# Optimization experiments

Hardware: AMD Instinct MI355X
Metric: run time of the kernel (lower is better)

The kernel has to match this reference:

```python
import jax, jax.numpy as jnp
import numpy as np

NUM_HOPS = 3

def _position_encoding(sentence_size, embedding_size):
    # Vectorized version of the double loop in the source.
    i = np.arange(1, embedding_size + 1, dtype=np.float32)[:, None]  # [E,1]
    j = np.arange(1, sentence_size + 1, dtype=np.float32)[None, :]   # [1,S]
    enc = (i - embedding_size / 2.0) * (j - sentence_size / 2.0)
    enc = 1.0 + 4.0 * enc / embedding_size / sentence_size
    return jnp.asarray(np.transpose(enc))  # [S, E]

def setup_inputs() -> dict:
    key = jax.random.key(0)
    ks = jax.random.split(key, 9)
    B, M, S, E, V, OUT = 16, 512, 32, 128, 32000, 128
    scale = 0.02
    return {
        "queries": jax.random.randint(ks[0], (B, S), 0, V, dtype=jnp.int32),
        "stories": jax.random.randint(ks[1], (B, M, S), 0, V, dtype=jnp.int32),
        "query_biases": jax.random.normal(ks[2], (V - 1, E), jnp.float32) * scale,
        "stories_biases": jax.random.normal(ks[3], (V - 1, E), jnp.float32) * scale,
        "memory_biases": jax.random.normal(ks[4], (M, E), jnp.float32) * scale,
        "output_biases": jax.random.normal(ks[5], (V - 1, E), jnp.float32) * scale,
        "w_intermediate": jax.random.normal(ks[6], (E, E), jnp.float32) * scale,
        "w_output": jax.random.normal(ks[7], (E, OUT), jnp.float32) * scale,
        "w_final": jax.random.normal(ks[8], (OUT, V), jnp.float32) * scale,
    }

def reference(queries, stories, query_biases, stories_biases, memory_biases,
              output_biases, w_intermediate, w_output, w_final):
    B, M, S = stories.shape
    E = query_biases.shape[1]
    enc = _position_encoding(S, E)  # [S, E]
    nil = jnp.zeros((1, E), dtype=query_biases.dtype)

    # Story memory: gather -> positional weight -> reduce over sentence axis.
    st_tab = jnp.concatenate([stories_biases, nil], axis=0)          # [V, E]
    mem_emb = st_tab[stories]                                        # [B,M,S,E]
    memory = jnp.einsum('bmse,se->bme', mem_emb, enc) + memory_biases

    # Query embedding.
    q_tab = jnp.concatenate([query_biases, nil], axis=0)
    q = jnp.einsum('bse,se->be', q_tab[queries], enc)                # [B,E]

    # Output memory.
    o_tab = jnp.concatenate([output_biases, nil], axis=0)
    output = jnp.einsum('bmse,se->bme', o_tab[stories], enc)         # [B,M,E]

    out_layer = q
    for hop in range(NUM_HOPS):
        probs = jax.nn.softmax(jnp.einsum('bme,be->bm', memory, q))  # [B,M]
        layer_out = jnp.einsum('bme,bm->be', output, probs)          # [B,E]
        w = w_output if hop == NUM_HOPS - 1 else w_intermediate
        out_layer = (q + layer_out) @ w
        q = out_layer                     # pre-nonlinearity state, as in source
        out_layer = jax.nn.relu(out_layer)

    return out_layer @ w_final            # [B, vocab]
```

## Files before the change

### kernel.cpp

```cpp
#include <hip/hip_runtime.h>

constexpr int kB  = 16;
constexpr int kM  = 512;
constexpr int kS  = 32;
constexpr int kE  = 128;
constexpr int kV  = 32000;
constexpr int kVN = kV - 1;

__global__ __launch_bounds__(256) void embed_stories_kernel(
    const int*   __restrict__ stories,
    const float* __restrict__ st_bias,
    const float* __restrict__ out_bias,
    const float* __restrict__ mem_bias,
    float*       __restrict__ memory,
    float*       __restrict__ output)
{
    __shared__ int sidx[2][kS];
    const int t     = threadIdx.x;
    const int pair0 = blockIdx.x * 2;
    if (t < 64) {
        const int p = t >> 5, s = t & 31;
        sidx[p][s] = stories[(pair0 + p) * kS + s];
    }
    __syncthreads();
    const int p  = t >> 7;
    const int e  = t & 127;
    const int bm = pair0 + p;
    const int m  = bm & (kM - 1);

    float accm = mem_bias[m * kE + e];
    float acco = 0.0f;
    const float ef = (float)(e - 63);
    #pragma unroll
    for (int s = 0; s < kS; ++s) {
        const int idx   = sidx[p][s];
        const float enc = 1.0f + ef * (float)(s - 15) * (1.0f / 1024.0f);
        if (idx < kVN) {
            const size_t off = (size_t)idx * kE + e;
            accm = fmaf(st_bias[off],  enc, accm);
            acco = fmaf(out_bias[off], enc, acco);
        }
    }
    memory[(size_t)bm * kE + e] = accm;
    output[(size_t)bm * kE + e] = acco;
}

__global__ __launch_bounds__(512) void hops_kernel(
    const int*   __restrict__ queries,
    const float* __restrict__ q_bias,
    const float* __restrict__ memory,
    const float* __restrict__ output,
    const float* __restrict__ w_int,
    const float* __restrict__ w_out,
    float*       __restrict__ x)
{
    __shared__ __align__(16) float q_s[kE];
    __shared__ float xbuf[kE];
    __shared__ float sc[kM];
    __shared__ float part[4][kE];
    __shared__ float red[8];
    __shared__ int   qidx[kS];

    const int b = blockIdx.x;
    const int t = threadIdx.x;

    if (t < kS) qidx[t] = queries[b * kS + t];
    __syncthreads();

    if (t < kE) {
        float acc = 0.0f;
        const float ef = (float)(t - 63);
        #pragma unroll
        for (int s = 0; s < kS; ++s) {
            const int idx   = qidx[s];
            const float enc = 1.0f + ef * (float)(s - 15) * (1.0f / 1024.0f);
            if (idx < kVN) acc = fmaf(q_bias[(size_t)idx * kE + t], enc, acc);
        }
        q_s[t] = acc;
    }
    __syncthreads();

    const float* memb = memory + (size_t)b * kM * kE;
    const float* outb = output + (size_t)b * kM * kE;
    const int g = t >> 7;
    const int e = t & 127;

    for (int hop = 0; hop < 3; ++hop) {
        const float4* row = (const float4*)(memb + (size_t)t * kE);
        const float4* qv  = (const float4*)q_s;
        float sv = 0.0f;
        #pragma unroll
        for (int i = 0; i < kE / 4; ++i) {
            const float4 a = row[i], q4 = qv[i];
            sv += a.x * q4.x + a.y * q4.y + a.z * q4.z + a.w * q4.w;
        }
        float v = sv;
        #pragma unroll
        for (int off = 32; off; off >>= 1) v = fmaxf(v, __shfl_down(v, off, 64));
        if ((t & 63) == 0) red[t >> 6] = v;
        __syncthreads();
        float mx = red[0];
        #pragma unroll
        for (int i = 1; i < 8; ++i) mx = fmaxf(mx, red[i]);
        const float ex = __expf(sv - mx);
        float sum = ex;
        #pragma unroll
        for (int off = 32; off; off >>= 1) sum += __shfl_down(sum, off, 64);
        __syncthreads();
        if ((t & 63) == 0) red[t >> 6] = sum;
        sc[t] = ex;
        __syncthreads();
        const float tot = red[0] + red[1] + red[2] + red[3] +
                          red[4] + red[5] + red[6] + red[7];
        const float inv = 1.0f / tot;

        float acc = 0.0f;
        const float* ob = outb + (size_t)g * 128 * kE;
        for (int mm = 0; mm < 128; ++mm)
            acc = fmaf(sc[g * 128 + mm], ob[(size_t)mm * kE + e], acc);
        part[g][e] = acc;
        __syncthreads();
        if (t < kE) {
            const float lo = (part[0][t] + part[1][t] + part[2][t] + part[3][t]) * inv;
            xbuf[t] = q_s[t] + lo;
        }
        __syncthreads();

        const float* w = (hop == 2) ? w_out : w_int;
        float acc2 = 0.0f;
        #pragma unroll 4
        for (int k = 0; k < 32; ++k) {
            const int ee = g * 32 + k;
            acc2 = fmaf(xbuf[ee], w[ee * kE + e], acc2);
        }
        part[g][e] = acc2;
        __syncthreads();
        if (t < kE) q_s[t] = part[0][t] + part[1][t] + part[2][t] + part[3][t];
        __syncthreads();
    }
    if (t < kE) x[b * kE + t] = fmaxf(q_s[t], 0.0f);
}

__global__ __launch_bounds__(256) void final_mm_kernel(
    const float* __restrict__ x,
    const float* __restrict__ wf,
    float*       __restrict__ out)
{
    __shared__ float xs[kB * kE];
    const int t = threadIdx.x;
    for (int i = t; i < kB * kE; i += 256) xs[i] = x[i];
    __syncthreads();

    const int v  = blockIdx.x * 256 + t;
    const int e0 = blockIdx.y * 32;
    float acc[kB];
    #pragma unroll
    for (int b = 0; b < kB; ++b) acc[b] = 0.0f;
    for (int e = e0; e < e0 + 32; ++e) {
        const float w = wf[(size_t)e * kV + v];
        #pragma unroll
        for (int b = 0; b < kB; ++b) acc[b] = fmaf(xs[b * kE + e], w, acc[b]);
    }
    #pragma unroll
    for (int b = 0; b < kB; ++b) atomicAdd(&out[(size_t)b * kV + v], acc[b]);
}

extern "C" void kernel_launch(void* const* d_in, const int* in_sizes, int n_in,
                              void* d_out, int out_size, void* d_ws, size_t ws_size,
                              hipStream_t stream)
{
    const int*   queries  = (const int*)  d_in[0];
    const int*   stories  = (const int*)  d_in[1];
    const float* q_bias   = (const float*)d_in[2];
    const float* st_bias  = (const float*)d_in[3];
    const float* mem_bias = (const float*)d_in[4];
    const float* out_bias = (const float*)d_in[5];
    const float* w_int    = (const float*)d_in[6];
    const float* w_out    = (const float*)d_in[7];
    const float* w_final  = (const float*)d_in[8];
    float* out = (float*)d_out;

    float* memory = (float*)d_ws;
    float* output = memory + (size_t)kB * kM * kE;
    float* x      = output + (size_t)kB * kM * kE;

    hipMemsetAsync(d_out, 0, (size_t)out_size * sizeof(float), stream);

    embed_stories_kernel<<<dim3((kB * kM) / 2), dim3(256), 0, stream>>>(
        stories, st_bias, out_bias, mem_bias, memory, output);

    hops_kernel<<<dim3(kB), dim3(512), 0, stream>>>(
        queries, q_bias, memory, output, w_int, w_out, x);

    final_mm_kernel<<<dim3(kV / 256, 4), dim3(256), 0, stream>>>(x, w_final, out);
}
```

Measured before the change: 186.2 us.

## Fuse hops and final matmul into one cooperative kernel; vectorize embedding gathers

The embedding kernel now has each warp gather float4 slices of eight sentence positions, with a shared-memory reduction across positions. The hops and final projection are merged into one cooperative launch of 256 blocks. Each of the 16 batches is computed redundantly by 16 blocks, a grid sync follows, and then each block computes 125 vocab columns over the full E dimension. This removes the memset, the atomics and one launch. The cost is redundant hop work, a grid-wide barrier, and a final matmul that uses only 125 of 256 threads per block.

```diff
diff --git a/kernel.cpp b/kernel.cpp
--- a/kernel.cpp
+++ b/kernel.cpp
@@ -1,4 +1,7 @@
 #include <hip/hip_runtime.h>
+#include <hip/hip_cooperative_groups.h>
+
+namespace cg = cooperative_groups;
 
 constexpr int kB  = 16;
 constexpr int kM  = 512;
@@ -16,153 +19,211 @@
     float*       __restrict__ output)
 {
     __shared__ int sidx[2][kS];
-    const int t     = threadIdx.x;
-    const int pair0 = blockIdx.x * 2;
-    if (t < 64) {
-        const int p = t >> 5, s = t & 31;
-        sidx[p][s] = stories[(pair0 + p) * kS + s];
-    }
-    __syncthreads();
-    const int p  = t >> 7;
+    __shared__ __align__(16) float pm[8][kE];
+    __shared__ __align__(16) float po[8][kE];
+
+    const int t    = threadIdx.x;
+    const int row0 = blockIdx.x * 2;
+    if (t < 64) sidx[t >> 5][t & 31] = stories[row0 * kS + t];
+    __syncthreads();
+
+    const int g    = t >> 5;
+    const int lane = t & 31;
+    const int p    = g >> 2;
+    const int ph   = g & 3;
+    const int e0   = lane * 4;
+    const float ef0 = (float)(e0 - 63), ef1 = (float)(e0 - 62);
+    const float ef2 = (float)(e0 - 61), ef3 = (float)(e0 - 60);
+
+    float4 am = {0.f, 0.f, 0.f, 0.f};
+    float4 ao = {0.f, 0.f, 0.f, 0.f};
+    #pragma unroll
+    for (int j = 0; j < 8; ++j) {
+        const int s   = ph * 8 + j;
+        const int idx = sidx[p][s];
+        const float sf = (float)(s - 15) * (1.0f / 1024.0f);
+        if (idx < kVN) {
+            const float4 vm = *(const float4*)(st_bias  + (size_t)idx * kE + e0);
+            const float4 vo = *(const float4*)(out_bias + (size_t)idx * kE + e0);
+            const float c0 = fmaf(ef0, sf, 1.0f), c1 = fmaf(ef1, sf, 1.0f);
+            const float c2 = fmaf(ef2, sf, 1.0f), c3 = fmaf(ef3, sf, 1.0f);
+            am.x = fmaf(vm.x, c0, am.x); am.y = fmaf(vm.y, c1, am.y);
+            am.z = fmaf(vm.z, c2, am.z); am.w = fmaf(vm.w, c3, am.w);
+            ao.x = fmaf(vo.x, c0, ao.x); ao.y = fmaf(vo.y, c1, ao.y);
+            ao.z = fmaf(vo.z, c2, ao.z); ao.w = fmaf(vo.w, c3, ao.w);
+        }
+    }
+    *(float4*)&pm[g][e0] = am;
+    *(float4*)&po[g][e0] = ao;
+    __syncthreads();
+
+    const int pr = t >> 7;
     const int e  = t & 127;
-    const int bm = pair0 + p;
-    const int m  = bm & (kM - 1);
-
-    float accm = mem_bias[m * kE + e];
-    float acco = 0.0f;
-    const float ef = (float)(e - 63);
-    #pragma unroll
-    for (int s = 0; s < kS; ++s) {
-        const int idx   = sidx[p][s];
-        const float enc = 1.0f + ef * (float)(s - 15) * (1.0f / 1024.0f);
-        if (idx < kVN) {
-            const size_t off = (size_t)idx * kE + e;
-            accm = fmaf(st_bias[off],  enc, accm);
-            acco = fmaf(out_bias[off], enc, acco);
-        }
-    }
-    memory[(size_t)bm * kE + e] = accm;
-    output[(size_t)bm * kE + e] = acco;
+    const int row = row0 + pr;
+    const int m   = row & (kM - 1);
+    const float sm = pm[pr * 4 + 0][e] + pm[pr * 4 + 1][e] +
+                     pm[pr * 4 + 2][e] + pm[pr * 4 + 3][e];
+    const float so = po[pr * 4 + 0][e] + po[pr * 4 + 1][e] +
+                     po[pr * 4 + 2][e] + po[pr * 4 + 3][e];
+    memory[(size_t)row * kE + e] = sm + mem_bias[m * kE + e];
+    output[(size_t)row * kE + e] = so;
 }
 
-__global__ __launch_bounds__(512) void hops_kernel(
+__global__ __launch_bounds__(256) void hops_final_kernel(
     const int*   __restrict__ queries,
     const float* __restrict__ q_bias,
     const float* __restrict__ memory,
     const float* __restrict__ output,
     const float* __restrict__ w_int,
     const float* __restrict__ w_out,
-    float*       __restrict__ x)
+    const float* __restrict__ w_final,
+    float*       __restrict__ xg,
+    float*       __restrict__ out)
 {
+    __shared__ int qidx[kS];
+    __shared__ __align__(16) float pq[8][kE];
     __shared__ __align__(16) float q_s[kE];
-    __shared__ float xbuf[kE];
-    __shared__ float sc[kM];
-    __shared__ float part[4][kE];
-    __shared__ float red[8];
-    __shared__ int   qidx[kS];
-
-    const int b = blockIdx.x;
-    const int t = threadIdx.x;
+    __shared__ float s_s[kM];
+    __shared__ __align__(16) float part2[2][kE];
+    __shared__ float xb[kE];
+    __shared__ float redA[4], redB[4];
+    __shared__ __align__(16) float xs[kB][kE];
+
+    cg::grid_group grid = cg::this_grid();
+    const int bid = blockIdx.x;
+    const int b   = bid & 15;
+    const int rep = bid >> 4;
+    const int t   = threadIdx.x;
 
     if (t < kS) qidx[t] = queries[b * kS + t];
     __syncthreads();
 
+    {
+        const int g = t >> 5, lane = t & 31, e0 = lane * 4;
+        const float ef0 = (float)(e0 - 63), ef1 = (float)(e0 - 62);
+        const float ef2 = (float)(e0 - 61), ef3 = (float)(e0 - 60);
+        float4 a = {0.f, 0.f, 0.f, 0.f};
+        #pragma unroll
+        for (int j = 0; j < 4; ++j) {
+            const int s   = g * 4 + j;
+            const int idx = qidx[s];
+            const float sf = (float)(s - 15) * (1.0f / 1024.0f);
+            if (idx < kVN) {
+                const float4 v = *(const float4*)(q_bias + (size_t)idx * kE + e0);
+                a.x = fmaf(v.x, fmaf(ef0, sf, 1.0f), a.x);
+                a.y = fmaf(v.y, fmaf(ef1, sf, 1.0f), a.y);
+                a.z = fmaf(v.z, fmaf(ef2, sf, 1.0f), a.z);
+                a.w = fmaf(v.w, fmaf(ef3, sf, 1.0f), a.w);
+            }
+        }
+        *(float4*)&pq[g][e0] = a;
+    }
+    __syncthreads();
     if (t < kE) {
-        float acc = 0.0f;
-        const float ef = (float)(t - 63);
-        #pragma unroll
-        for (int s = 0; s < kS; ++s) {
-            const int idx   = qidx[s];
-            const float enc = 1.0f + ef * (float)(s - 15) * (1.0f / 1024.0f);
-            if (idx < kVN) acc = fmaf(q_bias[(size_t)idx * kE + t], enc, acc);
-        }
-        q_s[t] = acc;
+        float s = 0.f;
+        #pragma unroll
+        for (int g = 0; g < 8; ++g) s += pq[g][t];
+        q_s[t] = s;
     }
     __syncthreads();
 
     const float* memb = memory + (size_t)b * kM * kE;
     const float* outb = output + (size_t)b * kM * kE;
-    const int g = t >> 7;
-    const int e = t & 127;
+    const int e    = t & 127;
+    const int half = t >> 7;
 
     for (int hop = 0; hop < 3; ++hop) {
-        const float4* row = (const float4*)(memb + (size_t)t * kE);
-        const float4* qv  = (const float4*)q_s;
-        float sv = 0.0f;
-        #pragma unroll
-        for (int i = 0; i < kE / 4; ++i) {
-            const float4 a = row[i], q4 = qv[i];
-            sv += a.x * q4.x + a.y * q4.y + a.z * q4.z + a.w * q4.w;
-        }
-        float v = sv;
-        #pragma unroll
-        for (int off = 32; off; off >>= 1) v = fmaxf(v, __shfl_down(v, off, 64));
-        if ((t & 63) == 0) red[t >> 6] = v;
-        __syncthreads();
-        float mx = red[0];
-        #pragma unroll
-        for (int i = 1; i < 8; ++i) mx = fmaxf(mx, red[i]);
-        const float ex = __expf(sv - mx);
-        float sum = ex;
-        #pragma unroll
-        for (int off = 32; off; off >>= 1) sum += __shfl_down(sum, off, 64);
-        __syncthreads();
-        if ((t & 63) == 0) red[t >> 6] = sum;
-        sc[t] = ex;
-        __syncthreads();
-        const float tot = red[0] + red[1] + red[2] + red[3] +
-                          red[4] + red[5] + red[6] + red[7];
-        const float inv = 1.0f / tot;
-
-        float acc = 0.0f;
-        const float* ob = outb + (size_t)g * 128 * kE;
-        for (int mm = 0; mm < 128; ++mm)
-            acc = fmaf(sc[g * 128 + mm], ob[(size_t)mm * kE + e], acc);
-        part[g][e] = acc;
-        __syncthreads();
-        if (t < kE) {
-            const float lo = (part[0][t] + part[1][t] + part[2][t] + part[3][t]) * inv;
-            xbuf[t] = q_s[t] + lo;
-        }
-        __syncthreads();
-
-        const float* w = (hop == 2) ? w_out : w_int;
-        float acc2 = 0.0f;
-        #pragma unroll 4
-        for (int k = 0; k < 32; ++k) {
-            const int ee = g * 32 + k;
-            acc2 = fmaf(xbuf[ee], w[ee * kE + e], acc2);
-        }
-        part[g][e] = acc2;
-        __syncthreads();
-        if (t < kE) q_s[t] = part[0][t] + part[1][t] + part[2][t] + part[3][t];
-        __syncthreads();
-    }
-    if (t < kE) x[b * kE + t] = fmaxf(q_s[t], 0.0f);
-}
-
-__global__ __launch_bounds__(256) void final_mm_kernel(
-    const float* __restrict__ x,
-    const float* __restrict__ wf,
-    float*       __restrict__ out)
-{
-    __shared__ float xs[kB * kE];
-    const int t = threadIdx.x;
-    for (int i = t; i < kB * kE; i += 256) xs[i] = x[i];
-    __syncthreads();
-
-    const int v  = blockIdx.x * 256 + t;
-    const int e0 = blockIdx.y * 32;
-    float acc[kB];
-    #pragma unroll
-    for (int b = 0; b < kB; ++b) acc[b] = 0.0f;
-    for (int e = e0; e < e0 + 32; ++e) {
-        const float w = wf[(size_t)e * kV + v];
-        #pragma unroll
-        for (int b = 0; b < kB; ++b) acc[b] = fmaf(xs[b * kE + e], w, acc[b]);
-    }
-    #pragma unroll
-    for (int b = 0; b < kB; ++b) atomicAdd(&out[(size_t)b * kV + v], acc[b]);
+        float sv0, sv1;
+        {
+            const float4* q4 = (const float4*)q_s;
+            const float4* r0 = (const float4*)(memb + (size_t)t * kE);
+            const float4* r1 = (const float4*)(memb + (size_t)(t + 256) * kE);
+            float a0 = 0.f, a1 = 0.f, b0 = 0.f, b1 = 0.f;
+            #pragma unroll 4
+            for (int i = 0; i < 32; i += 2) {
+                const float4 x0 = r0[i], y0 = r0[i + 1];
+                const float4 x1 = r1[i], y1 = r1[i + 1];
+                const float4 qa = q4[i], qb = q4[i + 1];
+                a0 = fmaf(x0.x, qa.x, a0); a0 = fmaf(x0.y, qa.y, a0);
+                a0 = fmaf(x0.z, qa.z, a0); a0 = fmaf(x0.w, qa.w, a0);
+                b0 = fmaf(y0.x, qb.x, b0); b0 = fmaf(y0.y, qb.y, b0);
+                b0 = fmaf(y0.z, qb.z, b0); b0 = fmaf(y0.w, qb.w, b0);
+                a1 = fmaf(x1.x, qa.x, a1); a1 = fmaf(x1.y, qa.y, a1);
+                a1 = fmaf(x1.z, qa.z, a1); a1 = fmaf(x1.w, qa.w, a1);
+                b1 = fmaf(y1.x, qb.x, b1); b1 = fmaf(y1.y, qb.y, b1);
+                b1 = fmaf(y1.z, qb.z, b1); b1 = fmaf(y1.w, qb.w, b1);
+            }
+            sv0 = a0 + b0; sv1 = a1 + b1;
+        }
+        float ml = fmaxf(sv0, sv1);
+        #pragma unroll
+        for (int off = 32; off; off >>= 1) ml = fmaxf(ml, __shfl_down(ml, off));
+        if ((t & 63) == 0) redA[t >> 6] = ml;
+        __syncthreads();
+        const float mx = fmaxf(fmaxf(redA[0], redA[1]), fmaxf(redA[2], redA[3]));
+        const float ex0 = __expf(sv0 - mx), ex1 = __expf(sv1 - mx);
+        float sl = ex0 + ex1;
+        #pragma unroll
+        for (int off = 32; off; off >>= 1) sl += __shfl_down(sl, off);
+        if ((t & 63) == 0) redB[t >> 6] = sl;
+        __syncthreads();
+        const float inv = 1.0f / (redB[0] + redB[1] + redB[2] + redB[3]);
+        s_s[t]       = ex0 * inv;
+        s_s[t + 256] = ex1 * inv;
+        __syncthreads();
+
+        {
+            const float* ob = outb + (size_t)half * 256 * kE + e;
+            const int mb = half * 256;
+            float a0 = 0.f, a1 = 0.f, a2 = 0.f, a3 = 0.f;
+            #pragma unroll 4
+            for (int m = 0; m < 256; m += 4) {
+                a0 = fmaf(s_s[mb + m + 0], ob[(size_t)(m + 0) * kE], a0);
+                a1 = fmaf(s_s[mb + m + 1], ob[(size_t)(m + 1) * kE], a1);
+                a2 = fmaf(s_s[mb + m + 2], ob[(size_t)(m + 2) * kE], a2);
+                a3 = fmaf(s_s[mb + m + 3], ob[(size_t)(m + 3) * kE], a3);
+            }
+            part2[half][e] = (a0 + a1) + (a2 + a3);
+        }
+        __syncthreads();
+        if (t < kE) xb[t] = q_s[t] + part2[0][t] + part2[1][t];
+        __syncthreads();
+
+        {
+            const float* w = (hop == 2) ? w_out : w_int;
+            float c0 = 0.f, c1 = 0.f;
+            #pragma unroll 8
+            for (int k = 0; k < 64; k += 2) {
+                const int kk = half * 64 + k;
+                c0 = fmaf(xb[kk],     w[(kk)     * kE + e], c0);
+                c1 = fmaf(xb[kk + 1], w[(kk + 1) * kE + e], c1);
+            }
+            part2[half][e] = c0 + c1;
+        }
+        __syncthreads();
+        if (t < kE) q_s[t] = part2[0][t] + part2[1][t];
+        __syncthreads();
+    }
+
+    if (rep == 0 && t < kE) xg[b * kE + t] = fmaxf(q_s[t], 0.f);
+    grid.sync();
+
+    for (int i = t; i < kB * kE; i += 256) xs[i >> 7][i & 127] = xg[i];
+    __syncthreads();
+    if (t < 125) {
+        const int v = bid * 125 + t;
+        float acc[kB];
+        #pragma unroll
+        for (int b2 = 0; b2 < kB; ++b2) acc[b2] = 0.f;
+        for (int e2 = 0; e2 < kE; ++e2) {
+            const float wv = w_final[(size_t)e2 * kV + v];
+            #pragma unroll
+            for (int b2 = 0; b2 < kB; ++b2)
+                acc[b2] = fmaf(xs[b2][e2], wv, acc[b2]);
+        }
+        #pragma unroll
+        for (int b2 = 0; b2 < kB; ++b2) out[(size_t)b2 * kV + v] = acc[b2];
+    }
 }
 
 extern "C" void kernel_launch(void* const* d_in, const int* in_sizes, int n_in,
@@ -182,15 +243,15 @@
 
     float* memory = (float*)d_ws;
     float* output = memory + (size_t)kB * kM * kE;
-    float* x      = output + (size_t)kB * kM * kE;
-
-    hipMemsetAsync(d_out, 0, (size_t)out_size * sizeof(float), stream);
+    float* xg     = output + (size_t)kB * kM * kE;
 
     embed_stories_kernel<<<dim3((kB * kM) / 2), dim3(256), 0, stream>>>(
         stories, st_bias, out_bias, mem_bias, memory, output);
 
-    hops_kernel<<<dim3(kB), dim3(512), 0, stream>>>(
-        queries, q_bias, memory, output, w_int, w_out, x);
-
-    final_mm_kernel<<<dim3(kV / 256, 4), dim3(256), 0, stream>>>(x, w_final, out);
+    void* args[] = {
+        (void*)&queries, (void*)&q_bias, (void*)&memory, (void*)&output,
+        (void*)&w_int, (void*)&w_out, (void*)&w_final, (void*)&xg, (void*)&out
+    };
+    hipLaunchCooperativeKernel((const void*)hops_final_kernel,
+                               dim3(256), dim3(256), args, 0, stream);
 }
```

Result: slower. 226.9 us (+21.8%).
